# Performance work log

Hardware: AMD Instinct MI355X
Metric: run time of the kernel (lower is better)

The kernel has to match this reference:

```python
import jax, jax.numpy as jnp
import numpy as np

B, S, T = 128, 512, 256


def setup_inputs() -> dict:
    key = jax.random.key(0)
    k1, k2, k3, k4 = jax.random.split(key, 4)
    emissions = jax.random.normal(k1, (B, S, T), dtype=jnp.float32)
    mask = jnp.ones((B, S), dtype=bool)
    transitions = jax.random.normal(k2, (T, T), dtype=jnp.float32)
    start_transitions = jax.random.normal(k3, (T,), dtype=jnp.float32)
    end_transitions = jax.random.normal(k4, (T,), dtype=jnp.float32)
    return {
        "emissions": emissions,
        "mask": mask,
        "transitions": transitions,
        "start_transitions": start_transitions,
        "end_transitions": end_transitions,
    }


def reference(emissions, mask, transitions, start_transitions, end_transitions):
    """Batched Viterbi decode. Returns (paths [B,S] int32, best_scores [B] f32).

    Faithful to CRFLayer._viterbi_decode: score_0 = start + em_0; at each step
    next[i,j] = score[i] + trans[i,j] + em_t[j], take max/argmax over i; add
    end_transitions at the end; backtrack via backpointers. Masked (padded)
    steps carry score through unchanged with identity backpointers, so padded
    tail positions replicate the last valid tag (mask is all-ones here, so
    output equals the original's full-length paths).
    """
    Bn, Sn, Tn = emissions.shape
    ident = jnp.arange(Tn, dtype=jnp.int32)
    score0 = start_transitions[None, :] + emissions[:, 0]  # [B,T]

    em_ts = jnp.swapaxes(emissions, 0, 1)[1:]  # [S-1,B,T]
    m_ts = jnp.swapaxes(mask, 0, 1)[1:]        # [S-1,B]

    def step(score, inp):
        em_t, m_t = inp
        # nxt[b,i,j] = score[b,i] + trans[i,j] + em_t[b,j]
        nxt = score[:, :, None] + transitions[None, :, :] + em_t[:, None, :]
        best = jnp.max(nxt, axis=1)                    # [B,T]
        idx = jnp.argmax(nxt, axis=1).astype(jnp.int32)  # [B,T] best prev tag
        m = m_t[:, None]
        new_score = jnp.where(m, best, score)
        bp = jnp.where(m, idx, ident[None, :])
        return new_score, bp

    final_score, history = jax.lax.scan(step, score0, (em_ts, m_ts))  # history [S-1,B,T]
    final_score = final_score + end_transitions[None, :]
    best_scores = jnp.max(final_score, axis=1)                         # [B]
    last_tag = jnp.argmax(final_score, axis=1).astype(jnp.int32)       # [B]

    def back(tag, hist_t):
        prev = jnp.take_along_axis(hist_t, tag[:, None], axis=1)[:, 0]
        return prev, tag  # carry prev tag, emit current tag

    first_tag, tags_rest = jax.lax.scan(back, last_tag, history, reverse=True)
    # tags_rest[t] = tag at position t+1; first_tag = tag at position 0
    paths = jnp.concatenate([first_tag[:, None], jnp.swapaxes(tags_rest, 0, 1)], axis=1)
    return paths, best_scores
```

## Files before the change

kernel.cpp:

```cpp
#include <hip/hip_runtime.h>

#define Bn 128
#define Sn 512
#define Tn 256
#define LPAD 320

template <int CTRL>
__device__ __forceinline__ float dpp_fmax(float v) {
  int x = __builtin_amdgcn_mov_dpp(__float_as_int(v), CTRL, 0xF, 0xF, true);
  return fmaxf(v, __int_as_float(x));
}
__device__ __forceinline__ float row_fmax16(float v) {
  v = dpp_fmax<0x128>(v);
  v = dpp_fmax<0x124>(v);
  v = dpp_fmax<0x122>(v);
  v = dpp_fmax<0x121>(v);
  return v;
}
__device__ __forceinline__ float wave_fmax64(float v) {
  v = row_fmax16(v);
  int x = __builtin_amdgcn_ds_swizzle(__float_as_int(v), 0x401F);
  v = fmaxf(v, __int_as_float(x));
  v = fmaxf(v, __shfl_xor(v, 32));
  return v;
}

__global__ __launch_bounds__(256) void transpose_kernel(
    const float* __restrict__ tr, float* __restrict__ trT) {
  int idx = blockIdx.x * 256 + threadIdx.x;
  int i = idx >> 8;
  int j = idx & 255;
  trT[j * Tn + i] = tr[i * Tn + j];
}

__global__ __launch_bounds__(1024, 4) void viterbi_fwd(
    const float* __restrict__ em,
    const float* __restrict__ trans,
    const float* __restrict__ start,
    float* __restrict__ scores)
{
  const int b    = blockIdx.x;
  const int tid  = threadIdx.x;
  const int lane = tid & 63;
  const int w    = tid >> 6;
  const int cg   = lane >> 4;
  const int ip   = lane & 15;
  const int jbase = w * 16 + cg * 4;
  const int i0    = ip * 16;
  const bool writer = (ip == 0);
  const int idxW = jbase + ((jbase >> 4) << 2);
  const int idxR = 20 * ip;

  __shared__ float sbuf[2][LPAD];

  float4 tr[16];
#pragma unroll
  for (int k = 0; k < 16; ++k)
    tr[k] = *reinterpret_cast<const float4*>(trans + (i0 + k) * Tn + jbase);

  const float* emb = em + (size_t)b * Sn * Tn;
  float* scb = scores + (size_t)b * Sn * Tn;

  if (tid < 64) {
    int j4 = tid * 4;
    float4 st = *reinterpret_cast<const float4*>(start + j4);
    float4 e0 = *reinterpret_cast<const float4*>(emb + j4);
    float4 s0 = make_float4(st.x + e0.x, st.y + e0.y, st.z + e0.z, st.w + e0.w);
    *reinterpret_cast<float4*>(&sbuf[0][j4 + ((tid >> 2) << 2)]) = s0;
    *reinterpret_cast<float4*>(scb + j4) = s0;
  }

  const float* emPre = emb + 2 * Tn + jbase;
  float* scW = scb + Tn + jbase;
  float4 eC;
  if (writer) eC = *reinterpret_cast<const float4*>(emb + Tn + jbase);
  float4 pA;
  float* pW = nullptr;
  __syncthreads();

  int cur = 0;
  for (int t = 1; t < Sn; ++t) {
    const float* sp = &sbuf[cur][idxR];
    float4 a0 = *reinterpret_cast<const float4*>(sp);
    float4 a1 = *reinterpret_cast<const float4*>(sp + 4);
    float4 a2 = *reinterpret_cast<const float4*>(sp + 8);
    float4 a3 = *reinterpret_cast<const float4*>(sp + 12);

    float4 eN;
    if (writer) {
      if (t > 1) *reinterpret_cast<float4*>(pW) = pA;
      const float* p = (t + 1 < Sn) ? emPre : emPre - Tn;
      eN = *reinterpret_cast<const float4*>(p);
    }

    float se[16] = {a0.x,a0.y,a0.z,a0.w, a1.x,a1.y,a1.z,a1.w,
                    a2.x,a2.y,a2.z,a2.w, a3.x,a3.y,a3.z,a3.w};

    float m0 = se[0] + tr[0].x;
    float m1 = se[0] + tr[0].y;
    float m2 = se[0] + tr[0].z;
    float m3 = se[0] + tr[0].w;
#pragma unroll
    for (int k = 1; k < 15; k += 2) {
      m0 = fmaxf(fmaxf(m0, se[k]+tr[k].x), se[k+1]+tr[k+1].x);
      m1 = fmaxf(fmaxf(m1, se[k]+tr[k].y), se[k+1]+tr[k+1].y);
      m2 = fmaxf(fmaxf(m2, se[k]+tr[k].z), se[k+1]+tr[k+1].z);
      m3 = fmaxf(fmaxf(m3, se[k]+tr[k].w), se[k+1]+tr[k+1].w);
    }
    m0 = fmaxf(m0, se[15]+tr[15].x);
    m1 = fmaxf(m1, se[15]+tr[15].y);
    m2 = fmaxf(m2, se[15]+tr[15].z);
    m3 = fmaxf(m3, se[15]+tr[15].w);

    m0 = row_fmax16(m0);
    m1 = row_fmax16(m1);
    m2 = row_fmax16(m2);
    m3 = row_fmax16(m3);

    if (writer) {
      float4 ns = make_float4(m0 + eC.x, m1 + eC.y, m2 + eC.z, m3 + eC.w);
      *reinterpret_cast<float4*>(&sbuf[cur ^ 1][idxW]) = ns;
      pA = ns; pW = scW;
      eC = eN;
    }
    emPre += Tn;
    scW   += Tn;
    cur ^= 1;
    __syncthreads();
  }
  if (writer) *reinterpret_cast<float4*>(pW) = pA;
}

__global__ __launch_bounds__(64) void viterbi_bwd(
    const float* __restrict__ em,
    const float* __restrict__ trT,
    const float* __restrict__ endt,
    const float* __restrict__ scores,
    float* __restrict__ out)
{
  const int b = blockIdx.x;
  const int lane = threadIdx.x;
  const float* scb = scores + (size_t)b * Sn * Tn;
  const float* emb = em + (size_t)b * Sn * Tn;
  const int base = lane * 4;
  const int BIG = 1 << 30;

  float4 s = *reinterpret_cast<const float4*>(scb + (size_t)(Sn - 1) * Tn + base);
  float4 e = *reinterpret_cast<const float4*>(endt + base);
  float d0 = s.x + e.x, d1 = s.y + e.y, d2 = s.z + e.z, d3 = s.w + e.w;
  float bv = fmaxf(fmaxf(fmaxf(d0, d1), d2), d3);
  bv = wave_fmax64(bv);
  int li = BIG;
  if (d3 == bv) li = base + 3;
  if (d2 == bv) li = base + 2;
  if (d1 == bv) li = base + 1;
  if (d0 == bv) li = base;
  unsigned long long mk = __ballot(li != BIG);
  int fl = (int)__ffsll(mk) - 1;
  int tag = __shfl(li, fl);
  if (lane == 0) {
    out[Bn * Sn + b] = bv;
    out[b * Sn + (Sn - 1)] = (float)tag;
  }

  float4 sv  = *reinterpret_cast<const float4*>(scb + (size_t)(Sn - 2) * Tn + base);
  float4 sv2 = *reinterpret_cast<const float4*>(scb + (size_t)(Sn - 3) * Tn + base);
  float4 e4  = *reinterpret_cast<const float4*>(emb + (size_t)(Sn - 1) * Tn + base);
  float4 e42 = *reinterpret_cast<const float4*>(emb + (size_t)(Sn - 2) * Tn + base);

  for (int k = Sn - 2; k >= 0; --k) {
    float4 tv = *reinterpret_cast<const float4*>(trT + (size_t)tag * Tn + base);
    int kp = (k >= 2) ? k - 2 : 0;
    int ke = (k >= 1) ? k - 1 : 0;
    float4 sv_nn = *reinterpret_cast<const float4*>(scb + (size_t)kp * Tn + base);
    float4 e4_nn = *reinterpret_cast<const float4*>(emb + (size_t)ke * Tn + base);

    int comp = tag & 3, src = tag >> 2;
    float es = (comp == 0) ? e4.x : (comp == 1) ? e4.y
             : (comp == 2) ? e4.z : e4.w;
    float ev = __shfl(es, src);

    d0 = (sv.x + tv.x) + ev;
    d1 = (sv.y + tv.y) + ev;
    d2 = (sv.z + tv.z) + ev;
    d3 = (sv.w + tv.w) + ev;
    bv = fmaxf(fmaxf(fmaxf(d0, d1), d2), d3);
    bv = wave_fmax64(bv);
    li = BIG;
    if (d3 == bv) li = base + 3;
    if (d2 == bv) li = base + 2;
    if (d1 == bv) li = base + 1;
    if (d0 == bv) li = base;
    mk = __ballot(li != BIG);
    fl = (int)__ffsll(mk) - 1;
    tag = __shfl(li, fl);
    if (lane == 0) out[b * Sn + k] = (float)tag;
    sv = sv2; sv2 = sv_nn;
    e4 = e42; e42 = e4_nn;
  }
}

extern "C" void kernel_launch(void* const* d_in, const int* in_sizes, int n_in,
                              void* d_out, int out_size, void* d_ws, size_t ws_size,
                              hipStream_t stream) {
  const float* em    = (const float*)d_in[0];
  const float* trans = (const float*)d_in[2];
  const float* start = (const float*)d_in[3];
  const float* endt  = (const float*)d_in[4];
  float* out = (float*)d_out;

  float* scores = (float*)d_ws;
  float* trT = (float*)((char*)d_ws + (size_t)Bn * Sn * Tn * 4);

  transpose_kernel<<<Tn * Tn / 256, 256, 0, stream>>>(trans, trT);
  viterbi_fwd<<<Bn, 1024, 0, stream>>>(em, trans, start, scores);
  viterbi_bwd<<<Bn, 64, 0, stream>>>(em, trT, endt, scores, out);
}
```

Before: 763.2 us.

## Interleave four batches per backtrack wave and pack forward max into v2f adds

The backward kernel now runs four independent batch backtracks in one wave, so the latency of each step's dependent gather and reductions can be hidden by the other chains. Tags are buffered in LDS and written out at the end, and the transposed transition matrix is pre-read once to warm the cache. The forward kernel reorganises its transition tile per output column so the score+transition adds can use packed two-wide float ops. In exchange the backward grid shrinks to 32 blocks, so fewer CUs are used and each wave carries more registers.

After: 1.351 ms. +77.0%, slower.

```diff
diff --git a/kernel.cpp b/kernel.cpp
--- a/kernel.cpp
+++ b/kernel.cpp
@@ -4,6 +4,9 @@
 #define Sn 512
 #define Tn 256
 #define LPAD 320
+#define PB 4
+
+typedef float v2f __attribute__((ext_vector_type(2)));
 
 template <int CTRL>
 __device__ __forceinline__ float dpp_fmax(float v) {
@@ -53,10 +56,13 @@
 
   __shared__ float sbuf[2][LPAD];
 
-  float4 tr[16];
-#pragma unroll
-  for (int k = 0; k < 16; ++k)
-    tr[k] = *reinterpret_cast<const float4*>(trans + (i0 + k) * Tn + jbase);
+  float trTile[4][16];
+#pragma unroll
+  for (int k = 0; k < 16; ++k) {
+    float4 r = *reinterpret_cast<const float4*>(trans + (i0 + k) * Tn + jbase);
+    trTile[0][k] = r.x; trTile[1][k] = r.y;
+    trTile[2][k] = r.z; trTile[3][k] = r.w;
+  }
 
   const float* emb = em + (size_t)b * Sn * Tn;
   float* scb = scores + (size_t)b * Sn * Tn;
@@ -93,32 +99,38 @@
       eN = *reinterpret_cast<const float4*>(p);
     }
 
-    float se[16] = {a0.x,a0.y,a0.z,a0.w, a1.x,a1.y,a1.z,a1.w,
-                    a2.x,a2.y,a2.z,a2.w, a3.x,a3.y,a3.z,a3.w};
-
-    float m0 = se[0] + tr[0].x;
-    float m1 = se[0] + tr[0].y;
-    float m2 = se[0] + tr[0].z;
-    float m3 = se[0] + tr[0].w;
-#pragma unroll
-    for (int k = 1; k < 15; k += 2) {
-      m0 = fmaxf(fmaxf(m0, se[k]+tr[k].x), se[k+1]+tr[k+1].x);
-      m1 = fmaxf(fmaxf(m1, se[k]+tr[k].y), se[k+1]+tr[k+1].y);
-      m2 = fmaxf(fmaxf(m2, se[k]+tr[k].z), se[k+1]+tr[k+1].z);
-      m3 = fmaxf(fmaxf(m3, se[k]+tr[k].w), se[k+1]+tr[k+1].w);
-    }
-    m0 = fmaxf(m0, se[15]+tr[15].x);
-    m1 = fmaxf(m1, se[15]+tr[15].y);
-    m2 = fmaxf(m2, se[15]+tr[15].z);
-    m3 = fmaxf(m3, se[15]+tr[15].w);
-
-    m0 = row_fmax16(m0);
-    m1 = row_fmax16(m1);
-    m2 = row_fmax16(m2);
-    m3 = row_fmax16(m3);
+    v2f se2[8];
+    se2[0] = (v2f){a0.x, a0.y}; se2[1] = (v2f){a0.z, a0.w};
+    se2[2] = (v2f){a1.x, a1.y}; se2[3] = (v2f){a1.z, a1.w};
+    se2[4] = (v2f){a2.x, a2.y}; se2[5] = (v2f){a2.z, a2.w};
+    se2[6] = (v2f){a3.x, a3.y}; se2[7] = (v2f){a3.z, a3.w};
+
+    float mc[4];
+#pragma unroll
+    for (int c = 0; c < 4; ++c) {
+      const v2f* tp = reinterpret_cast<const v2f*>(&trTile[c][0]);
+      v2f s0 = se2[0] + tp[0];
+      v2f s1 = se2[1] + tp[1];
+      v2f s2 = se2[2] + tp[2];
+      v2f s3 = se2[3] + tp[3];
+      v2f s4 = se2[4] + tp[4];
+      v2f s5 = se2[5] + tp[5];
+      v2f s6 = se2[6] + tp[6];
+      v2f s7 = se2[7] + tp[7];
+      float m = fmaxf(fmaxf(s0.x, s0.y), s1.x);
+      m = fmaxf(fmaxf(m, s1.y), s2.x);
+      m = fmaxf(fmaxf(m, s2.y), s3.x);
+      m = fmaxf(fmaxf(m, s3.y), s4.x);
+      m = fmaxf(fmaxf(m, s4.y), s5.x);
+      m = fmaxf(fmaxf(m, s5.y), s6.x);
+      m = fmaxf(fmaxf(m, s6.y), s7.x);
+      m = fmaxf(m, s7.y);
+      mc[c] = row_fmax16(m);
+    }
 
     if (writer) {
-      float4 ns = make_float4(m0 + eC.x, m1 + eC.y, m2 + eC.z, m3 + eC.w);
+      float4 ns = make_float4(mc[0] + eC.x, mc[1] + eC.y,
+                              mc[2] + eC.z, mc[3] + eC.w);
       *reinterpret_cast<float4*>(&sbuf[cur ^ 1][idxW]) = ns;
       pA = ns; pW = scW;
       eC = eN;
@@ -131,72 +143,123 @@
   if (writer) *reinterpret_cast<float4*>(pW) = pA;
 }
 
-__global__ __launch_bounds__(64) void viterbi_bwd(
+__global__ __launch_bounds__(64, 1) void viterbi_bwd(
     const float* __restrict__ em,
     const float* __restrict__ trT,
     const float* __restrict__ endt,
     const float* __restrict__ scores,
     float* __restrict__ out)
 {
-  const int b = blockIdx.x;
+  const int wb = blockIdx.x;
   const int lane = threadIdx.x;
-  const float* scb = scores + (size_t)b * Sn * Tn;
-  const float* emb = em + (size_t)b * Sn * Tn;
   const int base = lane * 4;
   const int BIG = 1 << 30;
 
-  float4 s = *reinterpret_cast<const float4*>(scb + (size_t)(Sn - 1) * Tn + base);
+  __shared__ unsigned char pbuf[PB][Sn];
+
+  float warm = 0.0f;
+  for (int off = base; off < Tn * Tn; off += 256) {
+    float4 wv = *reinterpret_cast<const float4*>(trT + off);
+    warm += wv.x + wv.y + wv.z + wv.w;
+  }
+  warm *= 0.0f;
+
+  const float* scb[PB];
+  const float* emb[PB];
+  int tags[PB];
   float4 e = *reinterpret_cast<const float4*>(endt + base);
-  float d0 = s.x + e.x, d1 = s.y + e.y, d2 = s.z + e.z, d3 = s.w + e.w;
-  float bv = fmaxf(fmaxf(fmaxf(d0, d1), d2), d3);
-  bv = wave_fmax64(bv);
-  int li = BIG;
-  if (d3 == bv) li = base + 3;
-  if (d2 == bv) li = base + 2;
-  if (d1 == bv) li = base + 1;
-  if (d0 == bv) li = base;
-  unsigned long long mk = __ballot(li != BIG);
-  int fl = (int)__ffsll(mk) - 1;
-  int tag = __shfl(li, fl);
-  if (lane == 0) {
-    out[Bn * Sn + b] = bv;
-    out[b * Sn + (Sn - 1)] = (float)tag;
-  }
-
-  float4 sv  = *reinterpret_cast<const float4*>(scb + (size_t)(Sn - 2) * Tn + base);
-  float4 sv2 = *reinterpret_cast<const float4*>(scb + (size_t)(Sn - 3) * Tn + base);
-  float4 e4  = *reinterpret_cast<const float4*>(emb + (size_t)(Sn - 1) * Tn + base);
-  float4 e42 = *reinterpret_cast<const float4*>(emb + (size_t)(Sn - 2) * Tn + base);
-
-  for (int k = Sn - 2; k >= 0; --k) {
-    float4 tv = *reinterpret_cast<const float4*>(trT + (size_t)tag * Tn + base);
-    int kp = (k >= 2) ? k - 2 : 0;
-    int ke = (k >= 1) ? k - 1 : 0;
-    float4 sv_nn = *reinterpret_cast<const float4*>(scb + (size_t)kp * Tn + base);
-    float4 e4_nn = *reinterpret_cast<const float4*>(emb + (size_t)ke * Tn + base);
-
-    int comp = tag & 3, src = tag >> 2;
-    float es = (comp == 0) ? e4.x : (comp == 1) ? e4.y
-             : (comp == 2) ? e4.z : e4.w;
-    float ev = __shfl(es, src);
-
-    d0 = (sv.x + tv.x) + ev;
-    d1 = (sv.y + tv.y) + ev;
-    d2 = (sv.z + tv.z) + ev;
-    d3 = (sv.w + tv.w) + ev;
-    bv = fmaxf(fmaxf(fmaxf(d0, d1), d2), d3);
+
+#pragma unroll
+  for (int p = 0; p < PB; ++p) {
+    int b = wb * PB + p;
+    scb[p] = scores + (size_t)b * Sn * Tn;
+    emb[p] = em + (size_t)b * Sn * Tn;
+    float4 s = *reinterpret_cast<const float4*>(scb[p] + (size_t)(Sn - 1) * Tn + base);
+    float d0 = (s.x + e.x) + warm;
+    float d1 = (s.y + e.y) + warm;
+    float d2 = (s.z + e.z) + warm;
+    float d3 = (s.w + e.w) + warm;
+    float bv = fmaxf(fmaxf(fmaxf(d0, d1), d2), d3);
     bv = wave_fmax64(bv);
-    li = BIG;
+    int li = BIG;
     if (d3 == bv) li = base + 3;
     if (d2 == bv) li = base + 2;
     if (d1 == bv) li = base + 1;
     if (d0 == bv) li = base;
-    mk = __ballot(li != BIG);
-    fl = (int)__ffsll(mk) - 1;
-    tag = __shfl(li, fl);
-    if (lane == 0) out[b * Sn + k] = (float)tag;
-    sv = sv2; sv2 = sv_nn;
-    e4 = e42; e42 = e4_nn;
+    unsigned long long mk = __ballot(li != BIG);
+    int fl = (int)__ffsll(mk) - 1;
+    int tag = __shfl(li, fl);
+    tags[p] = tag;
+    if (lane == 0) {
+      out[Bn * Sn + b] = bv;
+      pbuf[p][Sn - 1] = (unsigned char)tag;
+    }
+  }
+
+  float4 sv[PB], sv2[PB], e4[PB], e42[PB];
+#pragma unroll
+  for (int p = 0; p < PB; ++p) {
+    sv[p]  = *reinterpret_cast<const float4*>(scb[p] + (size_t)(Sn - 2) * Tn + base);
+    sv2[p] = *reinterpret_cast<const float4*>(scb[p] + (size_t)(Sn - 3) * Tn + base);
+    e4[p]  = *reinterpret_cast<const float4*>(emb[p] + (size_t)(Sn - 1) * Tn + base);
+    e42[p] = *reinterpret_cast<const float4*>(emb[p] + (size_t)(Sn - 2) * Tn + base);
+  }
+
+  for (int k = Sn - 2; k >= 0; --k) {
+    float4 tv[PB];
+#pragma unroll
+    for (int p = 0; p < PB; ++p)
+      tv[p] = *reinterpret_cast<const float4*>(trT + (size_t)tags[p] * Tn + base);
+
+    int kp = (k >= 2) ? k - 2 : 0;
+    int ke = (k >= 1) ? k - 1 : 0;
+    float4 svn[PB], e4n[PB];
+#pragma unroll
+    for (int p = 0; p < PB; ++p) {
+      svn[p] = *reinterpret_cast<const float4*>(scb[p] + (size_t)kp * Tn + base);
+      e4n[p] = *reinterpret_cast<const float4*>(emb[p] + (size_t)ke * Tn + base);
+    }
+
+    int nt[PB];
+#pragma unroll
+    for (int p = 0; p < PB; ++p) {
+      int comp = tags[p] & 3, src = tags[p] >> 2;
+      float es = (comp == 0) ? e4[p].x : (comp == 1) ? e4[p].y
+               : (comp == 2) ? e4[p].z : e4[p].w;
+      float ev = __shfl(es, src);
+      float d0 = (sv[p].x + tv[p].x) + ev;
+      float d1 = (sv[p].y + tv[p].y) + ev;
+      float d2 = (sv[p].z + tv[p].z) + ev;
+      float d3 = (sv[p].w + tv[p].w) + ev;
+      float bv = fmaxf(fmaxf(fmaxf(d0, d1), d2), d3);
+      bv = wave_fmax64(bv);
+      int li = BIG;
+      if (d3 == bv) li = base + 3;
+      if (d2 == bv) li = base + 2;
+      if (d1 == bv) li = base + 1;
+      if (d0 == bv) li = base;
+      unsigned long long mk = __ballot(li != BIG);
+      int fl = (int)__ffsll(mk) - 1;
+      nt[p] = __shfl(li, fl);
+    }
+
+    int tsel = (lane == 1) ? nt[1] : (lane == 2) ? nt[2]
+             : (lane == 3) ? nt[3] : nt[0];
+    if (lane < PB) pbuf[lane][k] = (unsigned char)tsel;
+
+#pragma unroll
+    for (int p = 0; p < PB; ++p) {
+      tags[p] = nt[p];
+      sv[p] = sv2[p]; sv2[p] = svn[p];
+      e4[p] = e42[p]; e42[p] = e4n[p];
+    }
+  }
+
+#pragma unroll
+  for (int p = 0; p < PB; ++p) {
+    int b = wb * PB + p;
+    for (int s = lane; s < Sn; s += 64)
+      out[(size_t)b * Sn + s] = (float)pbuf[p][s];
   }
 }
 
@@ -214,5 +277,5 @@
 
   transpose_kernel<<<Tn * Tn / 256, 256, 0, stream>>>(trans, trT);
   viterbi_fwd<<<Bn, 1024, 0, stream>>>(em, trans, start, scores);
-  viterbi_bwd<<<Bn, 64, 0, stream>>>(em, trT, endt, scores, out);
-}
+  viterbi_bwd<<<Bn / PB, 64, 0, stream>>>(em, trT, endt, scores, out);
+}
```

## Record per-tag group hints in forward pass to shortcut backward argmax

Applied to the files above, without the earlier changes.

The forward kernel changes its lane mapping so each wave reduces over source tags with shuffles. Along with each score it records a byte hint naming which 64-tag group holds the argmax predecessor. The backward kernel uses that hint to read one candidate per lane from the hinted group and finds the matching lane with a ballot, replacing the full 256-wide max reduction on the serial backtrack chain. It also preloads the transposed transition matrix into cache and buffers path tags in shared memory. The cost is an extra byte stream of hint writes and reads, plus more shuffle work in each forward step.

New measurement: 845.9 us. 1.11x slower.

```diff
diff --git a/kernel.cpp b/kernel.cpp
--- a/kernel.cpp
+++ b/kernel.cpp
@@ -3,7 +3,6 @@
 #define Bn 128
 #define Sn 512
 #define Tn 256
-#define LPAD 320
 
 template <int CTRL>
 __device__ __forceinline__ float dpp_fmax(float v) {
@@ -37,21 +36,24 @@
     const float* __restrict__ em,
     const float* __restrict__ trans,
     const float* __restrict__ start,
-    float* __restrict__ scores)
+    float* __restrict__ scores,
+    unsigned char* __restrict__ hints)
 {
   const int b    = blockIdx.x;
   const int tid  = threadIdx.x;
   const int lane = tid & 63;
   const int w    = tid >> 6;
-  const int cg   = lane >> 4;
-  const int ip   = lane & 15;
-  const int jbase = w * 16 + cg * 4;
+  const int ip   = lane >> 2;
+  const int jq   = lane & 3;
+  const int jbase = w * 16 + jq * 4;
   const int i0    = ip * 16;
-  const bool writer = (ip == 0);
-  const int idxW = jbase + ((jbase >> 4) << 2);
-  const int idxR = 20 * ip;
-
-  __shared__ float sbuf[2][LPAD];
+  const int b2 = ip & 1;
+  const int b3 = (ip >> 1) & 1;
+  const int a  = ip >> 2;
+  const int myc = jbase + b2 * 2 + b3;
+  const bool writer = (lane & 48) == 0;
+
+  __shared__ float sbuf[2][Tn];
 
   float4 tr[16];
 #pragma unroll
@@ -60,38 +62,37 @@
 
   const float* emb = em + (size_t)b * Sn * Tn;
   float* scb = scores + (size_t)b * Sn * Tn;
-
-  if (tid < 64) {
-    int j4 = tid * 4;
-    float4 st = *reinterpret_cast<const float4*>(start + j4);
-    float4 e0 = *reinterpret_cast<const float4*>(emb + j4);
+  unsigned char* hbw = hints + (size_t)b * Sn * Tn;
+
+  if (ip == 0) {
+    float4 st = *reinterpret_cast<const float4*>(start + jbase);
+    float4 e0 = *reinterpret_cast<const float4*>(emb + jbase);
     float4 s0 = make_float4(st.x + e0.x, st.y + e0.y, st.z + e0.z, st.w + e0.w);
-    *reinterpret_cast<float4*>(&sbuf[0][j4 + ((tid >> 2) << 2)]) = s0;
-    *reinterpret_cast<float4*>(scb + j4) = s0;
+    *reinterpret_cast<float4*>(&sbuf[0][jbase]) = s0;
+    *reinterpret_cast<float4*>(scb + jbase) = s0;
   }
 
   const float* emPre = emb + 2 * Tn + jbase;
-  float* scW = scb + Tn + jbase;
-  float4 eC;
-  if (writer) eC = *reinterpret_cast<const float4*>(emb + Tn + jbase);
-  float4 pA;
-  float* pW = nullptr;
+  float* scW = scb + Tn + myc;
+  unsigned char* hW = hbw + Tn + myc;
+  float4 eC = *reinterpret_cast<const float4*>(emb + Tn + jbase);
+  float pV = 0.0f;
+  unsigned char pG = 0;
+  float* pWd = nullptr;
+  unsigned char* pHd = nullptr;
   __syncthreads();
 
   int cur = 0;
   for (int t = 1; t < Sn; ++t) {
-    const float* sp = &sbuf[cur][idxR];
+    const float* sp = &sbuf[cur][i0];
     float4 a0 = *reinterpret_cast<const float4*>(sp);
     float4 a1 = *reinterpret_cast<const float4*>(sp + 4);
     float4 a2 = *reinterpret_cast<const float4*>(sp + 8);
     float4 a3 = *reinterpret_cast<const float4*>(sp + 12);
 
-    float4 eN;
-    if (writer) {
-      if (t > 1) *reinterpret_cast<float4*>(pW) = pA;
-      const float* p = (t + 1 < Sn) ? emPre : emPre - Tn;
-      eN = *reinterpret_cast<const float4*>(p);
-    }
+    if (writer && t > 1) { *pWd = pV; *pHd = pG; }
+    const float* p = (t + 1 < Sn) ? emPre : emPre - Tn;
+    float4 eN = *reinterpret_cast<const float4*>(p);
 
     float se[16] = {a0.x,a0.y,a0.z,a0.w, a1.x,a1.y,a1.z,a1.w,
                     a2.x,a2.y,a2.z,a2.w, a3.x,a3.y,a3.z,a3.w};
@@ -112,42 +113,78 @@
     m2 = fmaxf(m2, se[15]+tr[15].z);
     m3 = fmaxf(m3, se[15]+tr[15].w);
 
-    m0 = row_fmax16(m0);
-    m1 = row_fmax16(m1);
-    m2 = row_fmax16(m2);
-    m3 = row_fmax16(m3);
+    float d0 = m0 + eC.x;
+    float d1 = m1 + eC.y;
+    float d2 = m2 + eC.z;
+    float d3 = m3 + eC.w;
+
+    float sA = b2 ? d0 : d2;
+    float rA = __shfl_xor(sA, 4);
+    float sB = b2 ? d1 : d3;
+    float rB = __shfl_xor(sB, 4);
+    float p0 = fmaxf(b2 ? d2 : d0, rA);
+    float p1 = fmaxf(b2 ? d3 : d1, rB);
+    float sC = b3 ? p0 : p1;
+    float rC = __shfl_xor(sC, 8);
+    float q  = fmaxf(b3 ? p1 : p0, rC);
+
+    float q16 = __shfl_xor(q, 16);
+    bool tk3 = (q16 > q) || ((q16 == q) && (a & 1));
+    float qa = tk3 ? q16 : q;
+    int   ga = tk3 ? (a ^ 1) : a;
+
+    float q32 = __shfl_xor(qa, 32);
+    int   g32 = __shfl_xor(ga, 32);
+    bool tk4 = (q32 > qa) || ((q32 == qa) && (g32 < ga));
+    float qf = tk4 ? q32 : qa;
+    int   gf = tk4 ? g32 : ga;
 
     if (writer) {
-      float4 ns = make_float4(m0 + eC.x, m1 + eC.y, m2 + eC.z, m3 + eC.w);
-      *reinterpret_cast<float4*>(&sbuf[cur ^ 1][idxW]) = ns;
-      pA = ns; pW = scW;
-      eC = eN;
+      sbuf[cur ^ 1][myc] = qf;
+      pV = qf; pWd = scW;
+      pG = (unsigned char)gf; pHd = hW;
     }
+    eC = eN;
     emPre += Tn;
     scW   += Tn;
+    hW    += Tn;
     cur ^= 1;
     __syncthreads();
   }
-  if (writer) *reinterpret_cast<float4*>(pW) = pA;
-}
-
-__global__ __launch_bounds__(64) void viterbi_bwd(
+  if (writer) { *pWd = pV; *pHd = pG; }
+}
+
+__global__ __launch_bounds__(64, 1) void viterbi_bwd(
     const float* __restrict__ em,
     const float* __restrict__ trT,
     const float* __restrict__ endt,
     const float* __restrict__ scores,
+    const unsigned char* __restrict__ hints,
     float* __restrict__ out)
 {
   const int b = blockIdx.x;
   const int lane = threadIdx.x;
   const float* scb = scores + (size_t)b * Sn * Tn;
   const float* emb = em + (size_t)b * Sn * Tn;
+  const unsigned char* hb = hints + (size_t)b * Sn * Tn;
   const int base = lane * 4;
   const int BIG = 1 << 30;
 
+  __shared__ unsigned char pbuf[Sn];
+
+  float warm = 0.0f;
+  for (int off = base; off < Tn * Tn; off += 256) {
+    float4 wv = *reinterpret_cast<const float4*>(trT + off);
+    warm += wv.x + wv.y + wv.z + wv.w;
+  }
+  warm *= 0.0f;
+
   float4 s = *reinterpret_cast<const float4*>(scb + (size_t)(Sn - 1) * Tn + base);
   float4 e = *reinterpret_cast<const float4*>(endt + base);
-  float d0 = s.x + e.x, d1 = s.y + e.y, d2 = s.z + e.z, d3 = s.w + e.w;
+  float d0 = (s.x + e.x) + warm;
+  float d1 = (s.y + e.y) + warm;
+  float d2 = (s.z + e.z) + warm;
+  float d3 = (s.w + e.w) + warm;
   float bv = fmaxf(fmaxf(fmaxf(d0, d1), d2), d3);
   bv = wave_fmax64(bv);
   int li = BIG;
@@ -156,48 +193,68 @@
   if (d1 == bv) li = base + 1;
   if (d0 == bv) li = base;
   unsigned long long mk = __ballot(li != BIG);
-  int fl = (int)__ffsll(mk) - 1;
-  int tag = __shfl(li, fl);
+  int tag = __shfl(li, (int)__ffsll(mk) - 1);
   if (lane == 0) {
     out[Bn * Sn + b] = bv;
-    out[b * Sn + (Sn - 1)] = (float)tag;
-  }
-
-  float4 sv  = *reinterpret_cast<const float4*>(scb + (size_t)(Sn - 2) * Tn + base);
-  float4 sv2 = *reinterpret_cast<const float4*>(scb + (size_t)(Sn - 3) * Tn + base);
+    pbuf[Sn - 1] = (unsigned char)tag;
+  }
+
+  #define LD_SR(kk, v0, v1, v2, v3) {                         \
+    const float* _p = scb + (size_t)(kk) * Tn + lane;         \
+    v0 = _p[0]; v1 = _p[64]; v2 = _p[128]; v3 = _p[192]; }
+
+  float sP0, sP1, sP2, sP3;
+  float sv0, sv1, sv2, sv3;
+  float sB0, sB1, sB2, sB3;
+  LD_SR(Sn - 1, sP0, sP1, sP2, sP3);
+  LD_SR(Sn - 2, sv0, sv1, sv2, sv3);
+  LD_SR(Sn - 3, sB0, sB1, sB2, sB3);
   float4 e4  = *reinterpret_cast<const float4*>(emb + (size_t)(Sn - 1) * Tn + base);
-  float4 e42 = *reinterpret_cast<const float4*>(emb + (size_t)(Sn - 2) * Tn + base);
+  float4 e4B = *reinterpret_cast<const float4*>(emb + (size_t)(Sn - 2) * Tn + base);
+  unsigned int h1  = *reinterpret_cast<const unsigned int*>(hb + (size_t)(Sn - 1) * Tn + base);
+  unsigned int h1B = *reinterpret_cast<const unsigned int*>(hb + (size_t)(Sn - 2) * Tn + base);
 
   for (int k = Sn - 2; k >= 0; --k) {
-    float4 tv = *reinterpret_cast<const float4*>(trT + (size_t)tag * Tn + base);
+    const float* tp = trT + (size_t)tag * Tn + lane;
+    float tv0 = tp[0], tv1 = tp[64], tv2 = tp[128], tv3 = tp[192];
+
+    int hw = __shfl((int)h1, tag >> 2);
+    int g  = (hw >> ((tag & 3) * 8)) & 0xFF;
+
+    int cs = tag >> 6;
+    float sPs = (cs == 0) ? sP0 : (cs == 1) ? sP1 : (cs == 2) ? sP2 : sP3;
+    float dmax = __shfl(sPs, tag & 63);
+
+    int comp = tag & 3;
+    float es = (comp == 0) ? e4.x : (comp == 1) ? e4.y
+             : (comp == 2) ? e4.z : e4.w;
+    float ev = __shfl(es, tag >> 2);
+
     int kp = (k >= 2) ? k - 2 : 0;
     int ke = (k >= 1) ? k - 1 : 0;
-    float4 sv_nn = *reinterpret_cast<const float4*>(scb + (size_t)kp * Tn + base);
-    float4 e4_nn = *reinterpret_cast<const float4*>(emb + (size_t)ke * Tn + base);
-
-    int comp = tag & 3, src = tag >> 2;
-    float es = (comp == 0) ? e4.x : (comp == 1) ? e4.y
-             : (comp == 2) ? e4.z : e4.w;
-    float ev = __shfl(es, src);
-
-    d0 = (sv.x + tv.x) + ev;
-    d1 = (sv.y + tv.y) + ev;
-    d2 = (sv.z + tv.z) + ev;
-    d3 = (sv.w + tv.w) + ev;
-    bv = fmaxf(fmaxf(fmaxf(d0, d1), d2), d3);
-    bv = wave_fmax64(bv);
-    li = BIG;
-    if (d3 == bv) li = base + 3;
-    if (d2 == bv) li = base + 2;
-    if (d1 == bv) li = base + 1;
-    if (d0 == bv) li = base;
-    mk = __ballot(li != BIG);
-    fl = (int)__ffsll(mk) - 1;
-    tag = __shfl(li, fl);
-    if (lane == 0) out[b * Sn + k] = (float)tag;
-    sv = sv2; sv2 = sv_nn;
-    e4 = e42; e42 = e4_nn;
-  }
+    float sN0, sN1, sN2, sN3;
+    LD_SR(kp, sN0, sN1, sN2, sN3);
+    float4 e4N = *reinterpret_cast<const float4*>(emb + (size_t)ke * Tn + base);
+    unsigned int h1N = *reinterpret_cast<const unsigned int*>(hb + (size_t)ke * Tn + base);
+
+    float sV = (g == 0) ? sv0 : (g == 1) ? sv1 : (g == 2) ? sv2 : sv3;
+    float tV = (g == 0) ? tv0 : (g == 1) ? tv1 : (g == 2) ? tv2 : tv3;
+    float d = (sV + tV) + ev;
+    unsigned long long m2 = __ballot(d == dmax);
+    tag = g * 64 + ((int)__ffsll(m2) - 1);
+    if (lane == 0) pbuf[k] = (unsigned char)tag;
+
+    sP0 = sv0; sP1 = sv1; sP2 = sv2; sP3 = sv3;
+    sv0 = sB0; sv1 = sB1; sv2 = sB2; sv3 = sB3;
+    sB0 = sN0; sB1 = sN1; sB2 = sN2; sB3 = sN3;
+    e4 = e4B; e4B = e4N;
+    h1 = h1B; h1B = h1N;
+  }
+  #undef LD_SR
+
+  __syncthreads();
+  for (int s2 = lane; s2 < Sn; s2 += 64)
+    out[(size_t)b * Sn + s2] = (float)pbuf[s2];
 }
 
 extern "C" void kernel_launch(void* const* d_in, const int* in_sizes, int n_in,
@@ -209,10 +266,13 @@
   const float* endt  = (const float*)d_in[4];
   float* out = (float*)d_out;
 
+  const size_t scoresBytes = (size_t)Bn * Sn * Tn * 4;
   float* scores = (float*)d_ws;
-  float* trT = (float*)((char*)d_ws + (size_t)Bn * Sn * Tn * 4);
+  float* trT = (float*)((char*)d_ws + scoresBytes);
+  unsigned char* hints = (unsigned char*)((char*)d_ws + scoresBytes
+                                          + (size_t)Tn * Tn * 4);
 
   transpose_kernel<<<Tn * Tn / 256, 256, 0, stream>>>(trans, trT);
-  viterbi_fwd<<<Bn, 1024, 0, stream>>>(em, trans, start, scores);
-  viterbi_bwd<<<Bn, 64, 0, stream>>>(em, trT, endt, scores, out);
-}
+  viterbi_fwd<<<Bn, 1024, 0, stream>>>(em, trans, start, scores, hints);
+  viterbi_bwd<<<Bn, 64, 0, stream>>>(em, trT, endt, scores, hints, out);
+}
```
